# Kernel optimization log

Measured on AMD Instinct MI355X. Metric: run time of the kernel, lower is better.

## Reference

```python
import jax, jax.numpy as jnp
import numpy as np

T, N, C, S = 1600, 32, 512, 200
BLANK = 0
ALPHA = 0.5
NEG = -1e30  # finite stand-in for -inf (safe for grads)


def setup_inputs() -> dict:
    key = jax.random.key(0)
    k1, k2, k3 = jax.random.split(key, 3)
    # valid log-probabilities (log-softmax over vocab), shape (T, N, C)
    log_probs = jax.nn.log_softmax(jax.random.normal(k1, (T, N, C), jnp.float32), axis=-1)
    # labels in [1, C) so blank=0 never appears in targets
    targets = jax.random.randint(k2, (N, S), 1, C)
    input_lens = jnp.full((N,), T, dtype=jnp.int32)
    target_lens = jax.random.randint(k3, (N,), S // 2, S + 1)
    return {"log_probs": log_probs, "targets": targets,
            "input_lens": input_lens, "target_lens": target_lens}


def _ctc_forward(log_probs, targets, input_lens, target_lens):
    """Per-example CTC negative log-likelihood (reduction='none')."""
    Tt, Nn, Cc = log_probs.shape
    Ss = targets.shape[1]
    L = 2 * Ss + 1  # extended label sequence: blank, l1, blank, l2, ...

    ext = jnp.zeros((Nn, L), dtype=targets.dtype).at[:, 1::2].set(targets)  # (N, L)
    s_idx = jnp.arange(L)
    ext_m2 = jnp.pad(ext, ((0, 0), (2, 0)), constant_values=BLANK)[:, :L]
    # skip transition s-2 -> s allowed only for non-blank labels differing from s-2
    allow_skip = (ext != BLANK) & (ext != ext_m2) & (s_idx >= 2)[None, :]

    emit0 = jnp.take_along_axis(log_probs[0], ext, axis=1)  # (N, L)
    alpha0 = jnp.full((Nn, L), NEG, jnp.float32)
    alpha0 = alpha0.at[:, 0].set(emit0[:, 0])
    alpha0 = alpha0.at[:, 1].set(jnp.where(target_lens >= 1, emit0[:, 1], NEG))

    def step(alpha, xs):
        lp_t, t = xs  # lp_t: (N, C)
        emit = jnp.take_along_axis(lp_t, ext, axis=1)  # (N, L)
        a1 = jnp.pad(alpha, ((0, 0), (1, 0)), constant_values=NEG)[:, :L]
        a2 = jnp.where(allow_skip,
                       jnp.pad(alpha, ((0, 0), (2, 0)), constant_values=NEG)[:, :L],
                       NEG)
        m = jnp.maximum(jnp.maximum(alpha, a1), a2)
        new = m + jnp.log(jnp.exp(alpha - m) + jnp.exp(a1 - m) + jnp.exp(a2 - m)) + emit
        active = (t < input_lens)[:, None]  # freeze trellis past input_len
        return jnp.where(active, new, alpha), None

    alpha, _ = jax.lax.scan(step, alpha0, (log_probs[1:], jnp.arange(1, Tt)))

    idx_last = (2 * target_lens).astype(jnp.int32)  # final blank position
    idx_prev = jnp.maximum(idx_last - 1, 0)  # final label position
    a_last = jnp.take_along_axis(alpha, idx_last[:, None], axis=1)[:, 0]
    a_prev = jnp.where(target_lens > 0,
                       jnp.take_along_axis(alpha, idx_prev[:, None], axis=1)[:, 0],
                       NEG)
    return -jnp.logaddexp(a_last, a_prev)  # (N,)


def reference(log_probs, targets, input_lens, target_lens):
    per_ex = _ctc_forward(log_probs, targets, input_lens, target_lens)
    # zero_infinity=True: zero out infeasible alignments
    per_ex = jnp.where(per_ex < 1e29, per_ex, 0.0)
    norm = jnp.maximum(target_lens.astype(jnp.float32), 1.0) ** ALPHA
    return jnp.mean(per_ex / norm)
```

## Files before the change

### kernel.cpp

```cpp
#include <hip/hip_runtime.h>

#define T_DIM 1600
#define N_DIM 32
#define C_DIM 512
#define S_DIM 200
#define RCP_LN2 1.44269504088896340736f
#define LN2F 0.69314718055994530942f
#define ESENT (-(1 << 28))

static __device__ __forceinline__ float fast_exp2(float x) {
#if __has_builtin(__builtin_amdgcn_exp2f)
    return __builtin_amdgcn_exp2f(x);
#else
    return exp2f(x);
#endif
}

static __device__ __forceinline__ float fast_log2(float x) {
#if __has_builtin(__builtin_amdgcn_logf)
    return __builtin_amdgcn_logf(x);
#else
    return log2f(x);
#endif
}

static __device__ __forceinline__ float dpp_shr1_f(float x) {
    return __int_as_float(__builtin_amdgcn_update_dpp(
        0, __float_as_int(x), 0x138, 0xf, 0xf, false));
}
static __device__ __forceinline__ int dpp_shr1_i(int x, int old0) {
    return __builtin_amdgcn_update_dpp(old0, x, 0x138, 0xf, 0xf, false);
}
static __device__ __forceinline__ int dpp_prefix_max_i(int x) {
    int t;
    t = __builtin_amdgcn_update_dpp(x, x, 0x111, 0xf, 0xf, false); x = (t > x) ? t : x;
    t = __builtin_amdgcn_update_dpp(x, x, 0x112, 0xf, 0xf, false); x = (t > x) ? t : x;
    t = __builtin_amdgcn_update_dpp(x, x, 0x114, 0xf, 0xf, false); x = (t > x) ? t : x;
    t = __builtin_amdgcn_update_dpp(x, x, 0x118, 0xf, 0xf, false); x = (t > x) ? t : x;
    t = __builtin_amdgcn_update_dpp(x, x, 0x142, 0xf, 0xf, false); x = (t > x) ? t : x;
    t = __builtin_amdgcn_update_dpp(x, x, 0x143, 0xf, 0xf, false); x = (t > x) ? t : x;
    return x;
}

__global__ __launch_bounds__(128) void ctc_dp(
    const float* __restrict__ lp, const int* __restrict__ tgts,
    const int* __restrict__ input_lens, const int* __restrict__ target_lens,
    float* __restrict__ out)
{
    __shared__ float afin[512];
    __shared__ float bfin[512];
    __shared__ int escF[64];
    __shared__ int escB[64];

    const int n = blockIdx.x;
    const int tid = threadIdx.x;
    const int wid = tid >> 6;
    const int lane = tid & 63;
    const int* tgt = tgts + n * S_DIM;

    int len = input_lens[n];
    if (len > T_DIM) len = T_DIM;
    const int lenc = (len < 1) ? 1 : len;
    const int tl = target_lens[n];
    const int mid = (lenc + 1) >> 1;
    const int nsb = lenc - mid;

#define BOUNDARY() do {                                                       \
        float lm_ = fmaxf(fmaxf(fmaxf(a0, a1), fmaxf(a2, a3)),                \
                          fmaxf(fmaxf(a4, a5), fmaxf(a6, a7)));               \
        bool nz_ = (lm_ > 0.0f);                                              \
        int kl_ = (int)((__float_as_uint(lm_) >> 23) & 0xffu) - 127;          \
        int prop_ = nz_ ? (E + kl_) : ESENT;                                  \
        int g_ = dpp_prefix_max_i(prop_ + 32 * lane);                         \
        int Efin_ = g_ - 32 * lane;                                           \
        if (nz_) {                                                            \
            int sh_ = E - Efin_;                                              \
            int h1_ = sh_ / 2, h2_ = sh_ - h1_;                               \
            float f_ = fast_exp2((float)h1_), gg_ = fast_exp2((float)h2_);    \
            float fg_ = f_ * gg_;                                             \
            a0 *= fg_; a1 *= fg_; a2 *= fg_; a3 *= fg_;                       \
            a4 *= fg_; a5 *= fg_; a6 *= fg_; a7 *= fg_;                       \
        }                                                                     \
        int Eprev_ = dpp_shr1_i(Efin_, ESENT);                                \
        E = Efin_;                                                            \
        if (lane == 0) {                                                      \
            scale_d = 0.0f;                                                   \
        } else {                                                              \
            int d_ = Eprev_ - Efin_;               \
            scale_d = (d_ < -126) ? 0.0f : fast_exp2((float)d_);              \
        }                                                                     \
    } while (0)

    if (wid == 0) {
        int vo[4];
        float sk[4];
#pragma unroll
        for (int jj = 0; jj < 4; ++jj) {
            int s = lane * 8 + 2 * jj + 1;
            int i = (s - 1) >> 1;
            int lab = 0;
            float al = 0.0f;
            if (i < S_DIM) {
                lab = tgt[i];
                if (s >= 3 && i >= 1) al = (tgt[i] != tgt[i - 1]) ? 1.0f : 0.0f;
            }
            if (lab < 0 || lab >= C_DIM) lab = 0;
            vo[jj] = lab;
            sk[jj] = al;
        }

        float a0 = 0.0f, a1 = 0.0f, a2 = 0.0f, a3 = 0.0f;
        float a4 = 0.0f, a5 = 0.0f, a6 = 0.0f, a7 = 0.0f;
        int E = 0;
        float scale_d = (lane == 0) ? 0.0f : 1.0f;

        float lb[8], l1[8], l3[8], l5[8], l7[8];

#define LOADF(r_, ti_) do {                                                   \
            int tt_ = (ti_); if (tt_ > mid - 1) tt_ = mid - 1;                \
            const float* row_ = lp + ((size_t)tt_ * N_DIM + n) * C_DIM;       \
            lb[r_] = row_[0];                                                 \
            l1[r_] = row_[vo[0]];                                             \
            l3[r_] = row_[vo[1]];                                             \
            l5[r_] = row_[vo[2]];                                             \
            l7[r_] = row_[vo[3]];                                             \
        } while (0)

#pragma unroll
        for (int r = 0; r < 8; ++r) LOADF(r, r);

        const int ncf = (mid + 7) >> 3;
        for (int k = 0; k < ncf; ++k) {
            const int kb = k << 3;
#pragma unroll
            for (int r = 0; r < 8; ++r) {
                float pb_ = fast_exp2(lb[r] * RCP_LN2);
                float p1_ = fast_exp2(l1[r] * RCP_LN2);
                float p3_ = fast_exp2(l3[r] * RCP_LN2);
                float p5_ = fast_exp2(l5[r] * RCP_LN2);
                float p7_ = fast_exp2(l7[r] * RCP_LN2);
                LOADF(r, kb + r + 8);
                const int t_ = kb + r;
                if (t_ < mid) {
                    if (t_ == 0) {
                        if (lane == 0) {
                            a0 = pb_;
                            a1 = (tl >= 1) ? p1_ : 0.0f;
                        }
                    } else {
                        float P_ = dpp_shr1_f(a7) * scale_d;
                        float n0_ = (a0 + P_) * pb_;
                        float n1_ = fmaf(sk[0], P_,  a1 + a0) * p1_;
                        float n2_ = (a2 + a1) * pb_;
                        float n3_ = fmaf(sk[1], a1, a3 + a2) * p3_;
                        float n4_ = (a4 + a3) * pb_;
                        float n5_ = fmaf(sk[2], a3, a5 + a4) * p5_;
                        float n6_ = (a6 + a5) * pb_;
                        float n7_ = fmaf(sk[3], a5, a7 + a6) * p7_;
                        a0 = n0_; a1 = n1_; a2 = n2_; a3 = n3_;
                        a4 = n4_; a5 = n5_; a6 = n6_; a7 = n7_;
                    }
                }
            }
            BOUNDARY();
        }
#undef LOADF

        float4 lo = make_float4(a0, a1, a2, a3);
        float4 hi = make_float4(a4, a5, a6, a7);
        reinterpret_cast<float4*>(afin)[lane * 2] = lo;
        reinterpret_cast<float4*>(afin)[lane * 2 + 1] = hi;
        escF[lane] = E;
    } else {
        int vo[4];
        float aH[4];
#pragma unroll
        for (int jj = 0; jj < 4; ++jj) {
            int shat = lane * 8 + 2 * jj + 1;
            int s = 510 - shat;
            int lab = 0;
            float al = 0.0f;
            if (s >= 1 && s <= 399) {
                lab = tgt[(s - 1) >> 1];
                if (s + 2 <= 400) al = (tgt[(s + 1) >> 1] != tgt[(s - 1) >> 1]) ? 1.0f : 0.0f;
            }
            if (lab < 0 || lab >= C_DIM) lab = 0;
            vo[jj] = lab;
            aH[jj] = al;
        }

        float a0, a1, a2, a3, a4, a5, a6, a7;
#define BINIT(aj_, j_) do {                                                   \
            int s_ = 510 - (lane * 8 + (j_));                                 \
            aj_ = (s_ == 2 * tl || (tl > 0 && s_ == 2 * tl - 1)) ? 1.0f : 0.0f; \
        } while (0)
        BINIT(a0, 0); BINIT(a1, 1); BINIT(a2, 2); BINIT(a3, 3);
        BINIT(a4, 4); BINIT(a5, 5); BINIT(a6, 6); BINIT(a7, 7);
#undef BINIT
        int E = 0;
        float scale_d = (lane == 0) ? 0.0f : 1.0f;

        float lb[8], l1[8], l3[8], l5[8], l7[8];

#define LOADB(r_, ti_) do {                                                   \
            int tt_ = lenc - 1 - (ti_); if (tt_ < 0) tt_ = 0;                 \
            const float* row_ = lp + ((size_t)tt_ * N_DIM + n) * C_DIM;       \
            lb[r_] = row_[0];                                                 \
            l1[r_] = row_[vo[0]];                                             \
            l3[r_] = row_[vo[1]];                                             \
            l5[r_] = row_[vo[2]];                                             \
            l7[r_] = row_[vo[3]];                                             \
        } while (0)

#pragma unroll
        for (int r = 0; r < 8; ++r) LOADB(r, r);

        const int ncb = (nsb + 7) >> 3;
        for (int k = 0; k < ncb; ++k) {
            const int kb = k << 3;
#pragma unroll
            for (int r = 0; r < 8; ++r) {
                float pb_ = fast_exp2(lb[r] * RCP_LN2);
                float p1_ = fast_exp2(l1[r] * RCP_LN2);
                float p3_ = fast_exp2(l3[r] * RCP_LN2);
                float p5_ = fast_exp2(l5[r] * RCP_LN2);
                float p7_ = fast_exp2(l7[r] * RCP_LN2);
                LOADB(r, kb + r + 8);
                const int ti_ = kb + r;
                if (ti_ < nsb) {
                    float c0_ = pb_ * a0, c1_ = p1_ * a1;
                    float c2_ = pb_ * a2, c3_ = p3_ * a3;
                    float c4_ = pb_ * a4, c5_ = p5_ * a5;
                    float c6_ = pb_ * a6, c7_ = p7_ * a7;
                    float P_ = dpp_shr1_f(c7_) * scale_d;
                    a0 = c0_ + P_;
                    a1 = fmaf(aH[0], P_,  c1_ + c0_);
                    a2 = c2_ + c1_;
                    a3 = fmaf(aH[1], c1_, c3_ + c2_);
                    a4 = c4_ + c3_;
                    a5 = fmaf(aH[2], c3_, c5_ + c4_);
                    a6 = c6_ + c5_;
                    a7 = fmaf(aH[3], c5_, c7_ + c6_);
                }
            }
            BOUNDARY();
        }
#undef LOADB

        float4 lo = make_float4(a0, a1, a2, a3);
        float4 hi = make_float4(a4, a5, a6, a7);
        reinterpret_cast<float4*>(bfin)[lane * 2] = lo;
        reinterpret_cast<float4*>(bfin)[lane * 2 + 1] = hi;
        escB[lane] = E;
    }

    __syncthreads();

    if (tid < 64) {
        const int l = lane;
        const int Ef = escF[l];
        float m8 = -1e30f, s8 = 0.0f;
#pragma unroll
        for (int j = 0; j < 8; ++j) {
            int s = 8 * l + j;
            float x = -1e30f;
            if (s <= 400) {
                float af = afin[s];
                int shat = 510 - s;
                float bf = bfin[shat];
                if (af > 0.0f && bf > 0.0f)
                    x = fast_log2(af) + fast_log2(bf) + (float)(Ef + escB[shat >> 3]);
            }
            float m2 = fmaxf(m8, x);
            s8 = s8 * fast_exp2(m8 - m2) + fast_exp2(x - m2);
            m8 = m2;
        }
        float M = m8, V = s8;
#pragma unroll
        for (int off = 1; off < 64; off <<= 1) {
            float Mo = __shfl_xor(M, off);
            float Vo = __shfl_xor(V, off);
            float Mn = fmaxf(M, Mo);
            V = V * fast_exp2(M - Mn) + Vo * fast_exp2(Mo - Mn);
            M = Mn;
        }
        if (l == 0) {
            float X = M + fast_log2(V);
            float per_ex = -LN2F * X;
            if (!(per_ex < 1e29f)) per_ex = 0.0f;
            float tlf = (float)tl;
            if (tlf < 1.0f) tlf = 1.0f;
            atomicAdd(out, per_ex / sqrtf(tlf) * (1.0f / N_DIM));
        }
    }
#undef BOUNDARY
}

extern "C" void kernel_launch(void* const* d_in, const int* in_sizes, int n_in,
                              void* d_out, int out_size, void* d_ws, size_t ws_size,
                              hipStream_t stream) {
    (void)in_sizes; (void)n_in; (void)d_ws; (void)ws_size;
    const float* lp   = (const float*)d_in[0];
    const int* tgts   = (const int*)d_in[1];
    const int* ilens  = (const int*)d_in[2];
    const int* tlens  = (const int*)d_in[3];

    hipMemsetAsync(d_out, 0, (size_t)out_size * sizeof(float), stream);
    ctc_dp<<<N_DIM, 128, 0, stream>>>(lp, tgts, ilens, tlens, (float*)d_out);
}
```

Before: 273.5 us.

## Split forward and backward CTC passes into separate single-wave blocks

Each example's forward and backward DP waves now run in separate 64-thread blocks, giving 64 blocks, so the two directions can sit on different CUs and SIMDs rather than sharing one workgroup. Final alpha/beta states go to global workspace, and a per-example atomic counter lets the last-finishing block do the combine step. This spreads the serial DP across more hardware. The cost is an extra memset, global-memory round trips and fences for the combine.

```diff
diff --git a/kernel.cpp b/kernel.cpp
--- a/kernel.cpp
+++ b/kernel.cpp
@@ -42,20 +42,15 @@
     return x;
 }
 
-__global__ __launch_bounds__(128) void ctc_dp(
+__global__ __launch_bounds__(64) void ctc_dp(
     const float* __restrict__ lp, const int* __restrict__ tgts,
     const int* __restrict__ input_lens, const int* __restrict__ target_lens,
-    float* __restrict__ out)
+    float* __restrict__ out, float* __restrict__ ws)
 {
-    __shared__ float afin[512];
-    __shared__ float bfin[512];
-    __shared__ int escF[64];
-    __shared__ int escB[64];
-
-    const int n = blockIdx.x;
-    const int tid = threadIdx.x;
-    const int wid = tid >> 6;
-    const int lane = tid & 63;
+    const int blk = blockIdx.x;
+    const int n = blk >> 1;
+    const int role = blk & 1;
+    const int lane = threadIdx.x & 63;
     const int* tgt = tgts + n * S_DIM;
 
     int len = input_lens[n];
@@ -64,6 +59,12 @@
     const int tl = target_lens[n];
     const int mid = (lenc + 1) >> 1;
     const int nsb = lenc - mid;
+
+    float* afin_g = ws + 64 + (size_t)n * 1152;
+    float* bfin_g = afin_g + 512;
+    int* escF_g = (int*)(afin_g + 1024);
+    int* escB_g = escF_g + 64;
+    int* counter = (int*)ws + n;
 
 #define BOUNDARY() do {                                                       \
         float lm_ = fmaxf(fmaxf(fmaxf(a0, a1), fmaxf(a2, a3)),                \
@@ -91,7 +92,7 @@
         }                                                                     \
     } while (0)
 
-    if (wid == 0) {
+    if (role == 0) {
         int vo[4];
         float sk[4];
 #pragma unroll
@@ -168,9 +169,9 @@
 
         float4 lo = make_float4(a0, a1, a2, a3);
         float4 hi = make_float4(a4, a5, a6, a7);
-        reinterpret_cast<float4*>(afin)[lane * 2] = lo;
-        reinterpret_cast<float4*>(afin)[lane * 2 + 1] = hi;
-        escF[lane] = E;
+        reinterpret_cast<float4*>(afin_g)[lane * 2] = lo;
+        reinterpret_cast<float4*>(afin_g)[lane * 2 + 1] = hi;
+        escF_g[lane] = E;
     } else {
         int vo[4];
         float aH[4];
@@ -249,27 +250,35 @@
 
         float4 lo = make_float4(a0, a1, a2, a3);
         float4 hi = make_float4(a4, a5, a6, a7);
-        reinterpret_cast<float4*>(bfin)[lane * 2] = lo;
-        reinterpret_cast<float4*>(bfin)[lane * 2 + 1] = hi;
-        escB[lane] = E;
+        reinterpret_cast<float4*>(bfin_g)[lane * 2] = lo;
+        reinterpret_cast<float4*>(bfin_g)[lane * 2 + 1] = hi;
+        escB_g[lane] = E;
     }
 
-    __syncthreads();
-
-    if (tid < 64) {
+    __threadfence();
+    int prev = 0;
+    if (lane == 0)
+        prev = __hip_atomic_fetch_add(counter, 1, __ATOMIC_ACQ_REL,
+                                      __HIP_MEMORY_SCOPE_AGENT);
+    prev = __shfl(prev, 0);
+    if (prev != 1) return;
+
+    __threadfence();
+
+    {
         const int l = lane;
-        const int Ef = escF[l];
+        const int Ef = escF_g[l];
         float m8 = -1e30f, s8 = 0.0f;
 #pragma unroll
         for (int j = 0; j < 8; ++j) {
             int s = 8 * l + j;
             float x = -1e30f;
             if (s <= 400) {
-                float af = afin[s];
+                float af = afin_g[s];
                 int shat = 510 - s;
-                float bf = bfin[shat];
+                float bf = bfin_g[shat];
                 if (af > 0.0f && bf > 0.0f)
-                    x = fast_log2(af) + fast_log2(bf) + (float)(Ef + escB[shat >> 3]);
+                    x = fast_log2(af) + fast_log2(bf) + (float)(Ef + escB_g[shat >> 3]);
             }
             float m2 = fmaxf(m8, x);
             s8 = s8 * fast_exp2(m8 - m2) + fast_exp2(x - m2);
@@ -299,12 +308,14 @@
 extern "C" void kernel_launch(void* const* d_in, const int* in_sizes, int n_in,
                               void* d_out, int out_size, void* d_ws, size_t ws_size,
                               hipStream_t stream) {
-    (void)in_sizes; (void)n_in; (void)d_ws; (void)ws_size;
+    (void)in_sizes; (void)n_in; (void)ws_size;
     const float* lp   = (const float*)d_in[0];
     const int* tgts   = (const int*)d_in[1];
     const int* ilens  = (const int*)d_in[2];
     const int* tlens  = (const int*)d_in[3];
 
     hipMemsetAsync(d_out, 0, (size_t)out_size * sizeof(float), stream);
-    ctc_dp<<<N_DIM, 128, 0, stream>>>(lp, tgts, ilens, tlens, (float*)d_out);
-}
+    hipMemsetAsync(d_ws, 0, N_DIM * sizeof(int), stream);
+    ctc_dp<<<2 * N_DIM, 64, 0, stream>>>(lp, tgts, ilens, tlens,
+                                         (float*)d_out, (float*)d_ws);
+}
```

Measured after the change: 267.5 us. -2.2%, faster.
